# Kernel tuning notes

Measured on AMD Instinct MI355X. Metric: run time of the kernel, lower is better.

## Reference

```python
import jax, jax.numpy as jnp
import numpy as np

CONV_SPECS = [(1, 64, 4, 2), (64, 128, 8, 4), (128, 256, 10, 5), (256, 256, 12, 6)]  # (cin, cout, k, stride)
N_CODEBOOKS = 8
CODEBOOK_SIZE = 1024
D_MODEL = 256
STATE_FRAMES = 4
B = 8192


def setup_inputs() -> dict:
    key = jax.random.key(0)
    ks = jax.random.split(key, 3 + 2 * len(CONV_SPECS) + 1)
    d = {
        "audio_frame": jax.random.normal(ks[0], (B, 1, 240), dtype=jnp.float32),
        "state_in": jax.random.normal(ks[1], (B, D_MODEL, STATE_FRAMES), dtype=jnp.float32),
    }
    for i, (cin, cout, k, s) in enumerate(CONV_SPECS):
        scale = 1.0 / np.sqrt(cin * k)
        d[f"W{i}"] = jax.random.normal(ks[2 + 2 * i], (cout, cin, k), dtype=jnp.float32) * scale
        d[f"b{i}"] = jnp.zeros((cout,), dtype=jnp.float32)
    d["codebooks"] = jax.random.normal(ks[-1], (N_CODEBOOKS, CODEBOOK_SIZE, D_MODEL), dtype=jnp.float32) * 0.02
    return d


def _causal_conv(x, W, b, stride):
    # x: [B, Cin, L]; causal left-pad of (k - stride) so L_out = L // stride
    k = W.shape[-1]
    x = jnp.pad(x, ((0, 0), (0, 0), (k - stride, 0)))
    y = jax.lax.conv_general_dilated(
        x, W, window_strides=(stride,), padding="VALID",
        dimension_numbers=("NCH", "OIH", "NCH"))
    return y + b[None, :, None]


def _rvq_indices(x_btd, codebooks):
    # x_btd: [B, T, D]; codebooks: [Q, K, D] -> indices [B, Q, T]
    r = x_btd
    idxs = []
    for q in range(codebooks.shape[0]):
        cb = codebooks[q]                                        # [K, D]
        # ||r - c||^2 = ||r||^2 - 2 r.c + ||c||^2 ; ||r||^2 constant over k for argmin
        dist = jnp.sum(cb * cb, axis=-1) - 2.0 * jnp.einsum("btd,kd->btk", r, cb)
        idx = jnp.argmin(dist, axis=-1)                          # [B, T]
        r = r - cb[idx]                                          # residual update
        idxs.append(idx)
    return jnp.stack(idxs, axis=1)                               # [B, Q, T]


def reference(audio_frame, state_in, W0, b0, W1, b1, W2, b2, W3, b3, codebooks):
    # state: roll left, zero last frame
    new_state = jnp.roll(state_in, -1, axis=2).at[:, :, -1].set(0.0)

    # causal conv encoder stack (ELU between conv blocks)
    Ws, bs = (W0, W1, W2, W3), (b0, b1, b2, b3)
    x = audio_frame
    for i, (_, _, _, stride) in enumerate(CONV_SPECS):
        x = _causal_conv(x, Ws[i], bs[i], stride)
        if i < len(CONV_SPECS) - 1:
            x = jax.nn.elu(x)
    # x: [B, D_MODEL, 1]

    new_state = new_state.at[:, :, -1].set(x[:, :, -1])

    z = _rvq_indices(x.transpose(0, 2, 1), codebooks)            # [B, Q, T]
    acoustic_tokens = z[:, :, -1]                                # [B, 8]
    return acoustic_tokens, new_state
```

## Files before the change

### kernel.cpp

```cpp
#include <hip/hip_runtime.h>
#include <hip/hip_bf16.h>

#define GB 2

__device__ __forceinline__ float elu1(float v) { return v > 0.f ? v : expm1f(v); }

__global__ void cnorm_kernel(const float* __restrict__ cb, float* __restrict__ cnorm) {
    int g = blockIdx.x * blockDim.x + threadIdx.x;
    if (g >= 8 * 1024) return;
    const float* p = cb + (size_t)g * 256;
    float s = 0.f;
    for (int d = 0; d < 256; d += 4) {
        float4 v = *reinterpret_cast<const float4*>(p + d);
        s += v.x * v.x + v.y * v.y + v.z * v.z + v.w * v.w;
    }
    cnorm[g] = s;
}

__global__ void wtrans_kernel(const float* __restrict__ W1, const float* __restrict__ W2,
                              const float* __restrict__ W3, float* __restrict__ W1T,
                              float* __restrict__ W2T, float* __restrict__ W3T) {
    int g = blockIdx.x * blockDim.x + threadIdx.x;
    if (g < 8192) {
        int ci = g >> 7, c = g & 127;
        const float* src = W1 + c * 512 + ci * 8;
        float4 a = *reinterpret_cast<const float4*>(src);
        float4 b = *reinterpret_cast<const float4*>(src + 4);
        *reinterpret_cast<float4*>(W1T + g * 8) = a;
        *reinterpret_cast<float4*>(W1T + g * 8 + 4) = b;
    }
    int g2 = g - 8192;
    if (g2 >= 0 && g2 < 32768) {
        int ci = g2 >> 8, c = g2 & 255;
        const float* src = W2 + c * 1280 + ci * 10;
        float* dst = W2T + g2 * 10;
#pragma unroll
        for (int j = 0; j < 5; ++j)
            *reinterpret_cast<float2*>(dst + 2 * j) =
                *reinterpret_cast<const float2*>(src + 2 * j);
    }
    int g3 = g - 40960;
    if (g3 >= 0 && g3 < 65536) {
        int ci = g3 >> 8, c = g3 & 255;
        const float* src = W3 + c * 3072 + ci * 12 + 6;
        float* dst = W3T + g3 * 6;
#pragma unroll
        for (int j = 0; j < 3; ++j)
            *reinterpret_cast<float2*>(dst + 2 * j) =
                *reinterpret_cast<const float2*>(src + 2 * j);
    }
}

__global__ __launch_bounds__(256, 2)
void convA_kernel(const float* __restrict__ audio,
                  const float* __restrict__ W0, const float* __restrict__ b0,
                  const float* __restrict__ W1T, const float* __restrict__ b1,
                  float* __restrict__ y1g) {
    __shared__ __align__(16) float xs[244];
    __shared__ __align__(16) float y0s[64 * 124];

    const int tid = threadIdx.x;
    const int b = blockIdx.x;

    if (tid < 64) {
        y0s[tid * 124 + 0] = 0.f; y0s[tid * 124 + 1] = 0.f;
        y0s[tid * 124 + 2] = 0.f; y0s[tid * 124 + 3] = 0.f;
    }
    if (tid < 242) xs[tid] = (tid < 2) ? 0.f : audio[b * 240 + tid - 2];
    __syncthreads();
    {
        const int ci = tid >> 2, tg = tid & 3;
        float4 w = *reinterpret_cast<const float4*>(W0 + ci * 4);
        float bias = b0[ci];
        for (int t = tg; t < 120; t += 4) {
            float v = bias + w.x * xs[2 * t] + w.y * xs[2 * t + 1]
                           + w.z * xs[2 * t + 2] + w.w * xs[2 * t + 3];
            y0s[ci * 124 + 4 + t] = elu1(v);
        }
    }
    __syncthreads();
    {
        const int c = tid >> 1, half = tid & 1, t0 = 15 * half;
        float acc[15];
        float bias = b1[c];
#pragma unroll
        for (int u = 0; u < 15; ++u) acc[u] = bias;
        const float* wbase = W1T + c * 8;
        for (int ci = 0; ci < 64; ++ci) {
            float4 wA = *reinterpret_cast<const float4*>(wbase + ci * 1024);
            float4 wB = *reinterpret_cast<const float4*>(wbase + ci * 1024 + 4);
            const float* yb = y0s + ci * 124 + 4 * t0;
#pragma unroll
            for (int u = 0; u < 15; ++u) {
                float4 a = *reinterpret_cast<const float4*>(yb + 4 * u);
                float4 d = *reinterpret_cast<const float4*>(yb + 4 * u + 4);
                acc[u] += wA.x * a.x + wA.y * a.y + wA.z * a.z + wA.w * a.w
                        + wB.x * d.x + wB.y * d.y + wB.z * d.z + wB.w * d.w;
            }
        }
        float* yo = y1g + ((size_t)b * 128 + c) * 32 + t0;
#pragma unroll
        for (int u = 0; u < 15; ++u) yo[u] = elu1(acc[u]);
    }
}

__global__ __launch_bounds__(256, 2)
void convB_kernel(const float* __restrict__ state_in,
                  const float* __restrict__ b2, const float* __restrict__ b3,
                  const float* __restrict__ W2T, const float* __restrict__ W3T,
                  const float* __restrict__ y1g,
                  float* __restrict__ out, float* __restrict__ r_ws) {
    __shared__ __align__(16) float y1s[GB * 128 * 32];
    __shared__ __align__(16) float y2s[GB * 256 * 6];

    const int tid = threadIdx.x;
    const int bbase = blockIdx.x * GB;

    {
        const int col = tid & 31, grp = tid >> 5;
#pragma unroll
        for (int bi = 0; bi < GB; ++bi) {
            const float* src = y1g + ((size_t)(bbase + bi) * 128 + grp * 16) * 32 + col;
            float* dst = y1s + (bi * 128 + grp * 16) * 32 + col;
#pragma unroll
            for (int i = 0; i < 16; ++i) dst[i * 32] = src[i * 32];
        }
    }
    __syncthreads();
    {
        const int c = tid;
        float acc[GB][6];
        float bias = b2[c];
#pragma unroll
        for (int bi = 0; bi < GB; ++bi)
#pragma unroll
            for (int t = 0; t < 6; ++t) acc[bi][t] = bias;
        const float* wbase = W2T + c * 10;
        for (int ci = 0; ci < 128; ++ci) {
            float w[10];
#pragma unroll
            for (int jj = 0; jj < 5; ++jj) {
                float2 wv = *reinterpret_cast<const float2*>(wbase + ci * 2560 + jj * 2);
                w[jj * 2] = wv.x; w[jj * 2 + 1] = wv.y;
            }
#pragma unroll
            for (int bi = 0; bi < GB; ++bi) {
                const float* yr = y1s + (bi * 128 + ci) * 32;
                float row[32];
#pragma unroll
                for (int k4 = 0; k4 < 8; ++k4) {
                    float4 v = *reinterpret_cast<const float4*>(yr + k4 * 4);
                    row[k4 * 4] = v.x; row[k4 * 4 + 1] = v.y;
                    row[k4 * 4 + 2] = v.z; row[k4 * 4 + 3] = v.w;
                }
                acc[bi][0] += w[5] * row[0] + w[6] * row[1] + w[7] * row[2]
                            + w[8] * row[3] + w[9] * row[4];
#pragma unroll
                for (int t = 1; t < 6; ++t) {
                    const int q0 = 5 * t - 5;
                    float s = 0.f;
#pragma unroll
                    for (int j = 0; j < 10; ++j) s += w[j] * row[q0 + j];
                    acc[bi][t] += s;
                }
            }
        }
#pragma unroll
        for (int bi = 0; bi < GB; ++bi)
#pragma unroll
            for (int t = 0; t < 6; ++t)
                y2s[(bi * 256 + c) * 6 + t] = elu1(acc[bi][t]);
    }
    __syncthreads();
    {
        const int c = tid;
        float acc[GB];
        float bias = b3[c];
#pragma unroll
        for (int bi = 0; bi < GB; ++bi) acc[bi] = bias;
        const float* wbase = W3T + c * 6;
        for (int ci = 0; ci < 256; ++ci) {
            float2 w01 = *reinterpret_cast<const float2*>(wbase + ci * 1536);
            float2 w23 = *reinterpret_cast<const float2*>(wbase + ci * 1536 + 2);
            float2 w45 = *reinterpret_cast<const float2*>(wbase + ci * 1536 + 4);
#pragma unroll
            for (int bi = 0; bi < GB; ++bi) {
                const float* yr = y2s + (bi * 256 + ci) * 6;
                float2 a = *reinterpret_cast<const float2*>(yr);
                float2 d = *reinterpret_cast<const float2*>(yr + 2);
                float2 e = *reinterpret_cast<const float2*>(yr + 4);
                acc[bi] += w01.x * a.x + w01.y * a.y + w23.x * d.x + w23.y * d.y
                         + w45.x * e.x + w45.y * e.y;
            }
        }
#pragma unroll
        for (int bi = 0; bi < GB; ++bi) {
            const int b = bbase + bi;
            float y3 = acc[bi];
            r_ws[b * 256 + c] = y3;
            float4 si = *reinterpret_cast<const float4*>(state_in + b * 1024 + c * 4);
            float4 o; o.x = si.y; o.y = si.z; o.z = si.w; o.w = y3;
            *reinterpret_cast<float4*>(out + 65536 + b * 1024 + c * 4) = o;
        }
    }
}

__device__ __forceinline__ unsigned long long distkey(float d, int k) {
    unsigned u = __float_as_uint(d);
    u = (u & 0x80000000u) ? ~u : (u | 0x80000000u);
    return ((unsigned long long)u << 32) | (unsigned)k;
}

__global__ __launch_bounds__(512)
void rvq_kernel(const float* __restrict__ cb, const float* __restrict__ cnorm,
                const float* __restrict__ r_ws, float* __restrict__ out) {
    __shared__ __align__(16) float rs[32 * 256];
    __shared__ __align__(16) float cbs[16 * 1024];
    __shared__ unsigned long long part_sh[2][32];
    __shared__ int idx_sh[32];

    const int tid = threadIdx.x;
    const int lane = tid & 63;
    const int wid = tid >> 6;
    const int bg = wid >> 1;
    const int kg = wid & 1;
    const int b0 = blockIdx.x * 32;
    const int kbase = kg * 512 + 4 * lane;

    for (int it = 0; it < 4; ++it) {
        int o = (it * 512 + tid) * 4;
        *reinterpret_cast<float4*>(rs + o) =
            *reinterpret_cast<const float4*>(r_ws + b0 * 256 + o);
    }

    const int sk = tid >> 2;
    const int sdq = tid & 3;

    float v[8][4];
    {
        const float* src = cb + (size_t)sk * 256 + sdq * 4;
#pragma unroll
        for (int p = 0; p < 8; ++p) {
            float4 t = *reinterpret_cast<const float4*>(src + (size_t)p * 128 * 256);
            v[p][0] = t.x; v[p][1] = t.y; v[p][2] = t.z; v[p][3] = t.w;
        }
    }

    for (int q = 0; q < 8; ++q) {
        float acc[8][8];
#pragma unroll
        for (int i = 0; i < 8; ++i)
#pragma unroll
            for (int j = 0; j < 8; ++j) acc[i][j] = 0.f;

        for (int ds = 0; ds < 16; ++ds) {
            __syncthreads();
#pragma unroll
            for (int m = 0; m < 4; ++m) {
                const int d = sdq * 4 + m;
#pragma unroll
                for (int p = 0; p < 8; ++p) {
                    const int k = p * 128 + sk;
                    cbs[d * 1024 + ((k + 4 * d) & 1023)] = v[p][m];
                }
            }
            {
                int Sn = q * 16 + ds + 1; if (Sn > 127) Sn = 127;
                const int qn = Sn >> 4, dsn = Sn & 15;
                const float* src = cb + ((size_t)(qn * 1024 + sk)) * 256 + dsn * 16 + sdq * 4;
#pragma unroll
                for (int p = 0; p < 8; ++p) {
                    float4 t = *reinterpret_cast<const float4*>(src + (size_t)p * 128 * 256);
                    v[p][0] = t.x; v[p][1] = t.y; v[p][2] = t.z; v[p][3] = t.w;
                }
            }
            __syncthreads();
#pragma unroll
            for (int c4 = 0; c4 < 4; ++c4) {
                float rr[8][4];
#pragma unroll
                for (int i = 0; i < 8; ++i) {
                    float4 t = *reinterpret_cast<const float4*>(
                        rs + (bg * 8 + i) * 256 + ds * 16 + c4 * 4);
                    rr[i][0] = t.x; rr[i][1] = t.y; rr[i][2] = t.z; rr[i][3] = t.w;
                }
#pragma unroll
                for (int dd = 0; dd < 4; ++dd) {
                    const int dl = c4 * 4 + dd;
                    float4 cv0 = *reinterpret_cast<const float4*>(
                        cbs + dl * 1024 + ((kbase + 4 * dl) & 1023));
                    float4 cv1 = *reinterpret_cast<const float4*>(
                        cbs + dl * 1024 + ((kbase + 256 + 4 * dl) & 1023));
#pragma unroll
                    for (int i = 0; i < 8; ++i) {
                        const float r = rr[i][dd];
                        acc[i][0] += r * cv0.x; acc[i][1] += r * cv0.y;
                        acc[i][2] += r * cv0.z; acc[i][3] += r * cv0.w;
                        acc[i][4] += r * cv1.x; acc[i][5] += r * cv1.y;
                        acc[i][6] += r * cv1.z; acc[i][7] += r * cv1.w;
                    }
                }
            }
        }
        unsigned long long wkey[8];
#pragma unroll
        for (int i = 0; i < 8; ++i) wkey[i] = 0xFFFFFFFFFFFFFFFFull;
#pragma unroll
        for (int j = 0; j < 2; ++j) {
            float4 cn = *reinterpret_cast<const float4*>(
                cnorm + q * 1024 + kbase + 256 * j);
            float cne[4] = {cn.x, cn.y, cn.z, cn.w};
#pragma unroll
            for (int e = 0; e < 4; ++e) {
                const int kgl = kbase + 256 * j + e;
#pragma unroll
                for (int i = 0; i < 8; ++i) {
                    unsigned long long kk2 =
                        distkey(cne[e] - 2.f * acc[i][j * 4 + e], kgl);
                    if (kk2 < wkey[i]) wkey[i] = kk2;
                }
            }
        }
#pragma unroll
        for (int i = 0; i < 8; ++i) {
            unsigned long long k = wkey[i];
            for (int off = 32; off >= 1; off >>= 1) {
                unsigned long long o = __shfl_xor(k, off, 64);
                if (o < k) k = o;
            }
            if (lane == 0) part_sh[kg][bg * 8 + i] = k;
        }
        __syncthreads();
        if (tid < 32) {
            unsigned long long ka = part_sh[0][tid];
            unsigned long long kb = part_sh[1][tid];
            if (kb < ka) ka = kb;
            const int idx = (int)(ka & 0xFFFFFFFFu);
            idx_sh[tid] = idx;
            out[(b0 + tid) * 8 + q] = (float)idx;
        }
        __syncthreads();
        for (int it = 0; it < 16; ++it) {
            int flat = it * 512 + tid;
            int bL = flat >> 8, d = flat & 255;
            rs[bL * 256 + d] -= cb[((size_t)(q * 1024 + idx_sh[bL])) * 256 + d];
        }
    }
}

extern "C" void kernel_launch(void* const* d_in, const int* in_sizes, int n_in,
                              void* d_out, int out_size, void* d_ws, size_t ws_size,
                              hipStream_t stream) {
    const float* audio = (const float*)d_in[0];
    const float* state = (const float*)d_in[1];
    const float* W0 = (const float*)d_in[2];
    const float* b0 = (const float*)d_in[3];
    const float* W1 = (const float*)d_in[4];
    const float* b1 = (const float*)d_in[5];
    const float* W2 = (const float*)d_in[6];
    const float* b2 = (const float*)d_in[7];
    const float* W3 = (const float*)d_in[8];
    const float* b3 = (const float*)d_in[9];
    const float* cbk = (const float*)d_in[10];
    float* out = (float*)d_out;

    float* cnorm_ws = (float*)d_ws;
    float* r_ws = cnorm_ws + 8192;
    float* W1T = r_ws + 2097152;
    float* W2T = W1T + 65536;
    float* W3T = W2T + 327680;
    float* y1g = W3T + 393216;

    cnorm_kernel<<<32, 256, 0, stream>>>(cbk, cnorm_ws);
    wtrans_kernel<<<416, 256, 0, stream>>>(W1, W2, W3, W1T, W2T, W3T);
    convA_kernel<<<8192, 256, 0, stream>>>(audio, W0, b0, W1T, b1, y1g);
    convB_kernel<<<8192 / GB, 256, 0, stream>>>(state, b2, b3, W2T, W3T, y1g,
                                                out, r_ws);
    rvq_kernel<<<256, 512, 0, stream>>>(cbk, cnorm_ws, r_ws, out);
}
```

Baseline: 2.073 ms.

## Split fused conv2/conv3 kernel and halve RVQ block batch for more blocks

Splits the fused conv2+conv3 kernel into two kernels that pass intermediate activations through a workspace buffer, used only when the workspace is large enough. The conv3 stage then runs one batch per block with a per-block staging of activations, and conv2 gets a 2-blocks-per-CU launch bound. Separately, the RVQ kernel now handles 16 batch rows per block instead of 32 and splits the codebook across 4 wave groups instead of 2. This doubles the grid to 512 blocks and shrinks shared memory and accumulators. The aim is better occupancy and CU coverage, at the cost of extra global traffic for the intermediate activations and twice as many codebook passes overall.

New measurement: 2.484 ms. +19.8%, slower.

```diff
diff --git a/kernel.cpp b/kernel.cpp
--- a/kernel.cpp
+++ b/kernel.cpp
@@ -205,6 +205,115 @@
     }
 }
 
+__global__ __launch_bounds__(256, 2)
+void conv2_kernel(const float* __restrict__ b2, const float* __restrict__ W2T,
+                  const float* __restrict__ y1g, float* __restrict__ y2g) {
+    __shared__ __align__(16) float y1s[GB * 128 * 32];
+
+    const int tid = threadIdx.x;
+    const int bbase = blockIdx.x * GB;
+
+    {
+        const int col = tid & 31, grp = tid >> 5;
+#pragma unroll
+        for (int bi = 0; bi < GB; ++bi) {
+            const float* src = y1g + ((size_t)(bbase + bi) * 128 + grp * 16) * 32 + col;
+            float* dst = y1s + (bi * 128 + grp * 16) * 32 + col;
+#pragma unroll
+            for (int i = 0; i < 16; ++i) dst[i * 32] = src[i * 32];
+        }
+    }
+    __syncthreads();
+    {
+        const int c = tid;
+        float acc[GB][6];
+        float bias = b2[c];
+#pragma unroll
+        for (int bi = 0; bi < GB; ++bi)
+#pragma unroll
+            for (int t = 0; t < 6; ++t) acc[bi][t] = bias;
+        const float* wbase = W2T + c * 10;
+        for (int ci = 0; ci < 128; ++ci) {
+            float w[10];
+#pragma unroll
+            for (int jj = 0; jj < 5; ++jj) {
+                float2 wv = *reinterpret_cast<const float2*>(wbase + ci * 2560 + jj * 2);
+                w[jj * 2] = wv.x; w[jj * 2 + 1] = wv.y;
+            }
+#pragma unroll
+            for (int bi = 0; bi < GB; ++bi) {
+                const float* yr = y1s + (bi * 128 + ci) * 32;
+                float row[32];
+#pragma unroll
+                for (int k4 = 0; k4 < 8; ++k4) {
+                    float4 v = *reinterpret_cast<const float4*>(yr + k4 * 4);
+                    row[k4 * 4] = v.x; row[k4 * 4 + 1] = v.y;
+                    row[k4 * 4 + 2] = v.z; row[k4 * 4 + 3] = v.w;
+                }
+                acc[bi][0] += w[5] * row[0] + w[6] * row[1] + w[7] * row[2]
+                            + w[8] * row[3] + w[9] * row[4];
+#pragma unroll
+                for (int t = 1; t < 6; ++t) {
+                    const int q0 = 5 * t - 5;
+                    float s = 0.f;
+#pragma unroll
+                    for (int j = 0; j < 10; ++j) s += w[j] * row[q0 + j];
+                    acc[bi][t] += s;
+                }
+            }
+        }
+#pragma unroll
+        for (int bi = 0; bi < GB; ++bi) {
+            float* dst = y2g + ((size_t)(bbase + bi) * 256 + c) * 6;
+#pragma unroll
+            for (int jj = 0; jj < 3; ++jj) {
+                float2 o; o.x = elu1(acc[bi][jj * 2]); o.y = elu1(acc[bi][jj * 2 + 1]);
+                *reinterpret_cast<float2*>(dst + jj * 2) = o;
+            }
+        }
+    }
+}
+
+__global__ __launch_bounds__(256)
+void conv3_kernel(const float* __restrict__ state_in, const float* __restrict__ b3,
+                  const float* __restrict__ W3T, const float* __restrict__ y2g,
+                  float* __restrict__ out, float* __restrict__ r_ws) {
+    __shared__ __align__(16) float y2s[256 * 8];
+
+    const int tid = threadIdx.x;
+    const int b = blockIdx.x;
+
+    {
+        const float* src = y2g + ((size_t)b * 256 + tid) * 6;
+        float* dst = y2s + tid * 8;
+#pragma unroll
+        for (int jj = 0; jj < 3; ++jj)
+            *reinterpret_cast<float2*>(dst + jj * 2) =
+                *reinterpret_cast<const float2*>(src + jj * 2);
+    }
+    __syncthreads();
+    {
+        const int c = tid;
+        float acc = b3[c];
+        const float* wbase3 = W3T + c * 6;
+        for (int ci = 0; ci < 256; ++ci) {
+            float2 w01 = *reinterpret_cast<const float2*>(wbase3 + ci * 1536);
+            float2 w23 = *reinterpret_cast<const float2*>(wbase3 + ci * 1536 + 2);
+            float2 w45 = *reinterpret_cast<const float2*>(wbase3 + ci * 1536 + 4);
+            const float* yr = y2s + ci * 8;
+            float2 a = *reinterpret_cast<const float2*>(yr);
+            float2 d = *reinterpret_cast<const float2*>(yr + 2);
+            float2 e = *reinterpret_cast<const float2*>(yr + 4);
+            acc += w01.x * a.x + w01.y * a.y + w23.x * d.x + w23.y * d.y
+                 + w45.x * e.x + w45.y * e.y;
+        }
+        r_ws[b * 256 + c] = acc;
+        float4 si = *reinterpret_cast<const float4*>(state_in + b * 1024 + c * 4);
+        float4 o; o.x = si.y; o.y = si.z; o.z = si.w; o.w = acc;
+        *reinterpret_cast<float4*>(out + 65536 + b * 1024 + c * 4) = o;
+    }
+}
+
 __device__ __forceinline__ unsigned long long distkey(float d, int k) {
     unsigned u = __float_as_uint(d);
     u = (u & 0x80000000u) ? ~u : (u | 0x80000000u);
@@ -214,90 +323,83 @@
 __global__ __launch_bounds__(512)
 void rvq_kernel(const float* __restrict__ cb, const float* __restrict__ cnorm,
                 const float* __restrict__ r_ws, float* __restrict__ out) {
-    __shared__ __align__(16) float rs[32 * 256];
-    __shared__ __align__(16) float cbs[16 * 1024];
-    __shared__ unsigned long long part_sh[2][32];
-    __shared__ int idx_sh[32];
+    __shared__ __align__(16) float rs[16 * 256];
+    __shared__ __align__(16) float cbs[8 * 1024];
+    __shared__ unsigned long long part_sh[4][16];
+    __shared__ int idx_sh[16];
 
     const int tid = threadIdx.x;
     const int lane = tid & 63;
     const int wid = tid >> 6;
-    const int bg = wid >> 1;
-    const int kg = wid & 1;
-    const int b0 = blockIdx.x * 32;
-    const int kbase = kg * 512 + 4 * lane;
-
-    for (int it = 0; it < 4; ++it) {
+    const int bg = wid >> 2;
+    const int kg = wid & 3;
+    const int b0 = blockIdx.x * 16;
+    const int kbase = kg * 256 + 4 * lane;
+
+    for (int it = 0; it < 2; ++it) {
         int o = (it * 512 + tid) * 4;
         *reinterpret_cast<float4*>(rs + o) =
             *reinterpret_cast<const float4*>(r_ws + b0 * 256 + o);
     }
 
-    const int sk = tid >> 2;
-    const int sdq = tid & 3;
-
-    float v[8][4];
+    const int sk = tid >> 1;
+    const int sdq = tid & 1;
+
+    float v[4][4];
     {
         const float* src = cb + (size_t)sk * 256 + sdq * 4;
 #pragma unroll
-        for (int p = 0; p < 8; ++p) {
-            float4 t = *reinterpret_cast<const float4*>(src + (size_t)p * 128 * 256);
+        for (int p = 0; p < 4; ++p) {
+            float4 t = *reinterpret_cast<const float4*>(src + (size_t)p * 256 * 256);
             v[p][0] = t.x; v[p][1] = t.y; v[p][2] = t.z; v[p][3] = t.w;
         }
     }
 
     for (int q = 0; q < 8; ++q) {
-        float acc[8][8];
+        float acc[8][4];
 #pragma unroll
         for (int i = 0; i < 8; ++i)
 #pragma unroll
-            for (int j = 0; j < 8; ++j) acc[i][j] = 0.f;
-
-        for (int ds = 0; ds < 16; ++ds) {
+            for (int j = 0; j < 4; ++j) acc[i][j] = 0.f;
+
+        for (int ds = 0; ds < 32; ++ds) {
             __syncthreads();
 #pragma unroll
             for (int m = 0; m < 4; ++m) {
                 const int d = sdq * 4 + m;
 #pragma unroll
-                for (int p = 0; p < 8; ++p) {
-                    const int k = p * 128 + sk;
-                    cbs[d * 1024 + ((k + 4 * d) & 1023)] = v[p][m];
-                }
+                for (int p = 0; p < 4; ++p)
+                    cbs[d * 1024 + p * 256 + sk] = v[p][m];
             }
             {
-                int Sn = q * 16 + ds + 1; if (Sn > 127) Sn = 127;
-                const int qn = Sn >> 4, dsn = Sn & 15;
-                const float* src = cb + ((size_t)(qn * 1024 + sk)) * 256 + dsn * 16 + sdq * 4;
-#pragma unroll
-                for (int p = 0; p < 8; ++p) {
-                    float4 t = *reinterpret_cast<const float4*>(src + (size_t)p * 128 * 256);
+                int Sn = q * 32 + ds + 1; if (Sn > 255) Sn = 255;
+                const int qn = Sn >> 5, dsn = Sn & 31;
+                const float* src = cb + ((size_t)(qn * 1024 + sk)) * 256 + dsn * 8 + sdq * 4;
+#pragma unroll
+                for (int p = 0; p < 4; ++p) {
+                    float4 t = *reinterpret_cast<const float4*>(src + (size_t)p * 256 * 256);
                     v[p][0] = t.x; v[p][1] = t.y; v[p][2] = t.z; v[p][3] = t.w;
                 }
             }
             __syncthreads();
 #pragma unroll
-            for (int c4 = 0; c4 < 4; ++c4) {
+            for (int dp = 0; dp < 2; ++dp) {
                 float rr[8][4];
 #pragma unroll
                 for (int i = 0; i < 8; ++i) {
                     float4 t = *reinterpret_cast<const float4*>(
-                        rs + (bg * 8 + i) * 256 + ds * 16 + c4 * 4);
+                        rs + (bg * 8 + i) * 256 + ds * 8 + dp * 4);
                     rr[i][0] = t.x; rr[i][1] = t.y; rr[i][2] = t.z; rr[i][3] = t.w;
                 }
 #pragma unroll
                 for (int dd = 0; dd < 4; ++dd) {
-                    const int dl = c4 * 4 + dd;
-                    float4 cv0 = *reinterpret_cast<const float4*>(
-                        cbs + dl * 1024 + ((kbase + 4 * dl) & 1023));
-                    float4 cv1 = *reinterpret_cast<const float4*>(
-                        cbs + dl * 1024 + ((kbase + 256 + 4 * dl) & 1023));
+                    const int d = dp * 4 + dd;
+                    float4 cv = *reinterpret_cast<const float4*>(cbs + d * 1024 + kbase);
 #pragma unroll
                     for (int i = 0; i < 8; ++i) {
                         const float r = rr[i][dd];
-                        acc[i][0] += r * cv0.x; acc[i][1] += r * cv0.y;
-                        acc[i][2] += r * cv0.z; acc[i][3] += r * cv0.w;
-                        acc[i][4] += r * cv1.x; acc[i][5] += r * cv1.y;
-                        acc[i][6] += r * cv1.z; acc[i][7] += r * cv1.w;
+                        acc[i][0] += r * cv.x; acc[i][1] += r * cv.y;
+                        acc[i][2] += r * cv.z; acc[i][3] += r * cv.w;
                     }
                 }
             }
@@ -305,21 +407,17 @@
         unsigned long long wkey[8];
 #pragma unroll
         for (int i = 0; i < 8; ++i) wkey[i] = 0xFFFFFFFFFFFFFFFFull;
-#pragma unroll
-        for (int j = 0; j < 2; ++j) {
-            float4 cn = *reinterpret_cast<const float4*>(
-                cnorm + q * 1024 + kbase + 256 * j);
+        {
+            float4 cn = *reinterpret_cast<const float4*>(cnorm + q * 1024 + kbase);
             float cne[4] = {cn.x, cn.y, cn.z, cn.w};
 #pragma unroll
-            for (int e = 0; e < 4; ++e) {
-                const int kgl = kbase + 256 * j + e;
+            for (int e = 0; e < 4; ++e)
 #pragma unroll
                 for (int i = 0; i < 8; ++i) {
                     unsigned long long kk2 =
-                        distkey(cne[e] - 2.f * acc[i][j * 4 + e], kgl);
+                        distkey(cne[e] - 2.f * acc[i][e], kbase + e);
                     if (kk2 < wkey[i]) wkey[i] = kk2;
                 }
-            }
         }
 #pragma unroll
         for (int i = 0; i < 8; ++i) {
@@ -331,16 +429,17 @@
             if (lane == 0) part_sh[kg][bg * 8 + i] = k;
         }
         __syncthreads();
-        if (tid < 32) {
+        if (tid < 16) {
             unsigned long long ka = part_sh[0][tid];
-            unsigned long long kb = part_sh[1][tid];
-            if (kb < ka) ka = kb;
+            if (part_sh[1][tid] < ka) ka = part_sh[1][tid];
+            if (part_sh[2][tid] < ka) ka = part_sh[2][tid];
+            if (part_sh[3][tid] < ka) ka = part_sh[3][tid];
             const int idx = (int)(ka & 0xFFFFFFFFu);
             idx_sh[tid] = idx;
             out[(b0 + tid) * 8 + q] = (float)idx;
         }
         __syncthreads();
-        for (int it = 0; it < 16; ++it) {
+        for (int it = 0; it < 8; ++it) {
             int flat = it * 512 + tid;
             int bL = flat >> 8, d = flat & 255;
             rs[bL * 256 + d] -= cb[((size_t)(q * 1024 + idx_sh[bL])) * 256 + d];
@@ -370,11 +469,20 @@
     float* W2T = W1T + 65536;
     float* W3T = W2T + 327680;
     float* y1g = W3T + 393216;
+    float* y2g = y1g + 33554432;
+
+    const unsigned long long need_split = 49029120ull * 4ull;
+    const bool split = ws_size >= need_split;
 
     cnorm_kernel<<<32, 256, 0, stream>>>(cbk, cnorm_ws);
     wtrans_kernel<<<416, 256, 0, stream>>>(W1, W2, W3, W1T, W2T, W3T);
     convA_kernel<<<8192, 256, 0, stream>>>(audio, W0, b0, W1T, b1, y1g);
-    convB_kernel<<<8192 / GB, 256, 0, stream>>>(state, b2, b3, W2T, W3T, y1g,
-                                                out, r_ws);
-    rvq_kernel<<<256, 512, 0, stream>>>(cbk, cnorm_ws, r_ws, out);
-}
+    if (split) {
+        conv2_kernel<<<8192 / GB, 256, 0, stream>>>(b2, W2T, y1g, y2g);
+        conv3_kernel<<<8192, 256, 0, stream>>>(state, b3, W3T, y2g, out, r_ws);
+    } else {
+        convB_kernel<<<8192 / GB, 256, 0, stream>>>(state, b2, b3, W2T, W3T, y1g,
+                                                    out, r_ws);
+    }
+    rvq_kernel<<<512, 512, 0, stream>>>(cbk, cnorm_ws, r_ws, out);
+}
```

## Pre-transpose codebooks and stream them into LDS via async global_load_lds double buffering

Applied to the files above, without the earlier changes.

Adds a kernel that transposes the codebooks into d-major slabs of 8 dims by 1024 codes. The RVQ kernel now copies these slabs straight into a double-buffered LDS tile with global_load_lds, replacing the register-staged swizzled scatter. This removes the VGPR staging and the second barrier per step. Blocks shrink to 256 threads covering 16 rows each, so twice as many blocks launch with smaller shared memory. The argmin partials and indices now go through volatile global scratch instead of shared memory, which adds global-memory round trips and relies on the ordering of those volatile accesses.

Measured after the change: 2.354 ms. 13.6% more time.

```diff
diff --git a/kernel.cpp b/kernel.cpp
--- a/kernel.cpp
+++ b/kernel.cpp
@@ -15,6 +15,21 @@
         s += v.x * v.x + v.y * v.y + v.z * v.z + v.w * v.w;
     }
     cnorm[g] = s;
+}
+
+__global__ void cbtrans_kernel(const float* __restrict__ cb, float* __restrict__ cbT) {
+    int t = blockIdx.x * blockDim.x + threadIdx.x;
+    int o = t * 4;
+    const int s = o >> 13;
+    const int r = o & 8191;
+    const int dl = r >> 10;
+    const int k = r & 1023;
+    const int q = s >> 5;
+    const int d = (s & 31) * 8 + dl;
+    const float* src = cb + ((size_t)(q * 1024 + k)) * 256 + d;
+    float4 v;
+    v.x = src[0 * 256]; v.y = src[1 * 256]; v.z = src[2 * 256]; v.w = src[3 * 256];
+    *reinterpret_cast<float4*>(cbT + o) = v;
 }
 
 __global__ void wtrans_kernel(const float* __restrict__ W1, const float* __restrict__ W2,
@@ -211,40 +226,44 @@
     return ((unsigned long long)u << 32) | (unsigned)k;
 }
 
-__global__ __launch_bounds__(512)
-void rvq_kernel(const float* __restrict__ cb, const float* __restrict__ cnorm,
-                const float* __restrict__ r_ws, float* __restrict__ out) {
-    __shared__ __align__(16) float rs[32 * 256];
-    __shared__ __align__(16) float cbs[16 * 1024];
-    __shared__ unsigned long long part_sh[2][32];
-    __shared__ int idx_sh[32];
+#define RVQ_STAGE(S, BUF)                                                        \
+    {                                                                            \
+        _Pragma("unroll")                                                        \
+        for (int j = 0; j < 8; ++j) {                                            \
+            const int c_ = wid * 8 + j;          \
+            const float* g = cbT + (size_t)(S) * 8192 + c_ * 256 + lane * 4;     \
+            __builtin_amdgcn_global_load_lds(                                    \
+                (const __attribute__((address_space(1))) unsigned int*)g,        \
+                (__attribute__((address_space(3))) unsigned int*)                \
+                    (&cbs[BUF][0][0] + c_ * 256),                                \
+                16, 0, 0);                                                       \
+        }                                                                        \
+    }
+
+__global__ __launch_bounds__(256)
+void rvq_kernel(const float* __restrict__ cb, const float* __restrict__ cbT,
+                const float* __restrict__ cnorm, const float* __restrict__ r_ws,
+                float* __restrict__ out,
+                volatile unsigned long long* partg, volatile int* idxg) {
+    __shared__ __align__(16) float rs[16 * 256];
+    __shared__ __align__(16) float cbs[2][8][1024];
 
     const int tid = threadIdx.x;
     const int lane = tid & 63;
     const int wid = tid >> 6;
     const int bg = wid >> 1;
     const int kg = wid & 1;
-    const int b0 = blockIdx.x * 32;
-    const int kbase = kg * 512 + 4 * lane;
+    const int blk = blockIdx.x;
+    const int b0 = blk * 16;
+    const int kb = kg * 512 + 4 * lane;
 
     for (int it = 0; it < 4; ++it) {
-        int o = (it * 512 + tid) * 4;
+        int o = (it * 256 + tid) * 4;
         *reinterpret_cast<float4*>(rs + o) =
             *reinterpret_cast<const float4*>(r_ws + b0 * 256 + o);
     }
 
-    const int sk = tid >> 2;
-    const int sdq = tid & 3;
-
-    float v[8][4];
-    {
-        const float* src = cb + (size_t)sk * 256 + sdq * 4;
-#pragma unroll
-        for (int p = 0; p < 8; ++p) {
-            float4 t = *reinterpret_cast<const float4*>(src + (size_t)p * 128 * 256);
-            v[p][0] = t.x; v[p][1] = t.y; v[p][2] = t.z; v[p][3] = t.w;
-        }
-    }
+    RVQ_STAGE(0, 0)
 
     for (int q = 0; q < 8; ++q) {
         float acc[8][8];
@@ -253,44 +272,29 @@
 #pragma unroll
             for (int j = 0; j < 8; ++j) acc[i][j] = 0.f;
 
-        for (int ds = 0; ds < 16; ++ds) {
+        for (int ds = 0; ds < 32; ++ds) {
+            const int s = q * 32 + ds;
             __syncthreads();
-#pragma unroll
-            for (int m = 0; m < 4; ++m) {
-                const int d = sdq * 4 + m;
-#pragma unroll
-                for (int p = 0; p < 8; ++p) {
-                    const int k = p * 128 + sk;
-                    cbs[d * 1024 + ((k + 4 * d) & 1023)] = v[p][m];
-                }
-            }
             {
-                int Sn = q * 16 + ds + 1; if (Sn > 127) Sn = 127;
-                const int qn = Sn >> 4, dsn = Sn & 15;
-                const float* src = cb + ((size_t)(qn * 1024 + sk)) * 256 + dsn * 16 + sdq * 4;
-#pragma unroll
-                for (int p = 0; p < 8; ++p) {
-                    float4 t = *reinterpret_cast<const float4*>(src + (size_t)p * 128 * 256);
-                    v[p][0] = t.x; v[p][1] = t.y; v[p][2] = t.z; v[p][3] = t.w;
-                }
-            }
-            __syncthreads();
-#pragma unroll
-            for (int c4 = 0; c4 < 4; ++c4) {
+                int Sn = s + 1; if (Sn > 255) Sn = 255;
+                RVQ_STAGE(Sn, (s + 1) & 1)
+            }
+            const float* cbp = &cbs[s & 1][0][0];
+#pragma unroll
+            for (int dp = 0; dp < 2; ++dp) {
                 float rr[8][4];
 #pragma unroll
                 for (int i = 0; i < 8; ++i) {
                     float4 t = *reinterpret_cast<const float4*>(
-                        rs + (bg * 8 + i) * 256 + ds * 16 + c4 * 4);
+                        rs + (bg * 8 + i) * 256 + ds * 8 + dp * 4);
                     rr[i][0] = t.x; rr[i][1] = t.y; rr[i][2] = t.z; rr[i][3] = t.w;
                 }
 #pragma unroll
                 for (int dd = 0; dd < 4; ++dd) {
-                    const int dl = c4 * 4 + dd;
-                    float4 cv0 = *reinterpret_cast<const float4*>(
-                        cbs + dl * 1024 + ((kbase + 4 * dl) & 1023));
+                    const int dl = dp * 4 + dd;
+                    float4 cv0 = *reinterpret_cast<const float4*>(cbp + dl * 1024 + kb);
                     float4 cv1 = *reinterpret_cast<const float4*>(
-                        cbs + dl * 1024 + ((kbase + 256 + 4 * dl) & 1023));
+                        cbp + dl * 1024 + kb + 256);
 #pragma unroll
                     for (int i = 0; i < 8; ++i) {
                         const float r = rr[i][dd];
@@ -302,48 +306,42 @@
                 }
             }
         }
-        unsigned long long wkey[8];
-#pragma unroll
-        for (int i = 0; i < 8; ++i) wkey[i] = 0xFFFFFFFFFFFFFFFFull;
-#pragma unroll
-        for (int j = 0; j < 2; ++j) {
-            float4 cn = *reinterpret_cast<const float4*>(
-                cnorm + q * 1024 + kbase + 256 * j);
-            float cne[4] = {cn.x, cn.y, cn.z, cn.w};
-#pragma unroll
-            for (int e = 0; e < 4; ++e) {
-                const int kgl = kbase + 256 * j + e;
-#pragma unroll
-                for (int i = 0; i < 8; ++i) {
-                    unsigned long long kk2 =
-                        distkey(cne[e] - 2.f * acc[i][j * 4 + e], kgl);
-                    if (kk2 < wkey[i]) wkey[i] = kk2;
-                }
-            }
-        }
-#pragma unroll
-        for (int i = 0; i < 8; ++i) {
-            unsigned long long k = wkey[i];
-            for (int off = 32; off >= 1; off >>= 1) {
-                unsigned long long o = __shfl_xor(k, off, 64);
-                if (o < k) k = o;
-            }
-            if (lane == 0) part_sh[kg][bg * 8 + i] = k;
+        {
+            float4 cn0 = *reinterpret_cast<const float4*>(cnorm + q * 1024 + kb);
+            float4 cn1 = *reinterpret_cast<const float4*>(cnorm + q * 1024 + kb + 256);
+            float c0e[4] = {cn0.x, cn0.y, cn0.z, cn0.w};
+            float c1e[4] = {cn1.x, cn1.y, cn1.z, cn1.w};
+#pragma unroll
+            for (int i = 0; i < 8; ++i) {
+                unsigned long long k = 0xFFFFFFFFFFFFFFFFull;
+#pragma unroll
+                for (int e = 0; e < 4; ++e) {
+                    unsigned long long ka = distkey(c0e[e] - 2.f * acc[i][e], kb + e);
+                    unsigned long long kc = distkey(c1e[e] - 2.f * acc[i][4 + e],
+                                                    kb + 256 + e);
+                    if (ka < k) k = ka;
+                    if (kc < k) k = kc;
+                }
+                for (int off = 32; off >= 1; off >>= 1) {
+                    unsigned long long o = __shfl_xor(k, off, 64);
+                    if (o < k) k = o;
+                }
+                if (lane == 0) partg[blk * 32 + kg * 16 + bg * 8 + i] = k;
+            }
         }
         __syncthreads();
-        if (tid < 32) {
-            unsigned long long ka = part_sh[0][tid];
-            unsigned long long kb = part_sh[1][tid];
-            if (kb < ka) ka = kb;
+        if (tid < 16) {
+            unsigned long long ka = partg[blk * 32 + tid];
+            unsigned long long kc = partg[blk * 32 + 16 + tid];
+            if (kc < ka) ka = kc;
             const int idx = (int)(ka & 0xFFFFFFFFu);
-            idx_sh[tid] = idx;
+            idxg[blk * 16 + tid] = idx;
             out[(b0 + tid) * 8 + q] = (float)idx;
         }
         __syncthreads();
         for (int it = 0; it < 16; ++it) {
-            int flat = it * 512 + tid;
-            int bL = flat >> 8, d = flat & 255;
-            rs[bL * 256 + d] -= cb[((size_t)(q * 1024 + idx_sh[bL])) * 256 + d];
+            const int idx = idxg[blk * 16 + it];
+            rs[it * 256 + tid] -= cb[((size_t)(q * 1024 + idx)) * 256 + tid];
         }
     }
 }
@@ -370,11 +368,17 @@
     float* W2T = W1T + 65536;
     float* W3T = W2T + 327680;
     float* y1g = W3T + 393216;
+    float* cbT = y1g + 33554432;
+    float* extra = cbT + 2097152;
+
+    volatile unsigned long long* partg = (volatile unsigned long long*)extra;
+    volatile int* idxg = (volatile int*)(extra + 32768);
 
     cnorm_kernel<<<32, 256, 0, stream>>>(cbk, cnorm_ws);
+    cbtrans_kernel<<<2048, 256, 0, stream>>>(cbk, cbT);
     wtrans_kernel<<<416, 256, 0, stream>>>(W1, W2, W3, W1T, W2T, W3T);
     convA_kernel<<<8192, 256, 0, stream>>>(audio, W0, b0, W1T, b1, y1g);
     convB_kernel<<<8192 / GB, 256, 0, stream>>>(state, b2, b3, W2T, W3T, y1g,
                                                 out, r_ws);
-    rvq_kernel<<<256, 512, 0, stream>>>(cbk, cnorm_ws, r_ws, out);
-}
+    rvq_kernel<<<512, 256, 0, stream>>>(cbk, cbT, cnorm_ws, r_ws, out, partg, idxg);
+}
```
